# Optimization experiments

Measured on AMD Instinct MI355X. Metric: run time of the kernel, lower is better.

Reference implementation:

```python
import jax, jax.numpy as jnp
import numpy as np

B, C, HEADS, DH = 2, 1280, 20, 64
INNER = HEADS * DH
HW = 64
S = HW * HW
L = 77
ENC = 4096
GROUPS = 32
EPS = 1e-5
CREG = 1.0     # creg_ in __init__
NOATTN = 1.0   # global noattn
NORES = 1.0    # global noresidual


def setup_inputs() -> dict:
    key = jax.random.key(0)
    ks = jax.random.split(key, 10)
    std = 0.02
    return {
        "x": jax.random.normal(ks[0], (B, C, HW, HW), jnp.float32),
        "text": jax.random.normal(ks[1], (B, L, ENC), jnp.float32),
        "gn_gamma": jnp.ones((C,), jnp.float32),
        "gn_beta": jnp.zeros((C,), jnp.float32),
        "ln_gamma": jnp.ones((ENC,), jnp.float32),
        "ln_beta": jnp.zeros((ENC,), jnp.float32),
        "Wq": jax.random.normal(ks[2], (C, INNER), jnp.float32) * std,
        "bq": jnp.zeros((INNER,), jnp.float32),
        "Wk": jax.random.normal(ks[3], (ENC, INNER), jnp.float32) * std,
        "bk": jnp.zeros((INNER,), jnp.float32),
        "Wv": jax.random.normal(ks[4], (ENC, INNER), jnp.float32) * std,
        "bv": jnp.zeros((INNER,), jnp.float32),
        "Wo": jax.random.normal(ks[5], (INNER, C), jnp.float32) * std,
        "bo": jnp.zeros((C,), jnp.float32),
        "size_reg": jax.random.uniform(ks[6], (1, S, L), jnp.float32),
        "treg": jax.random.uniform(ks[7], (1,), jnp.float32),
        "mask": jax.random.randint(ks[8], (1, S, L), 0, 2, jnp.int32),
    }


def _group_norm(h, gamma, beta):
    # h: [B, C, S]; GroupNorm over (C//GROUPS, S) per group
    hg = h.reshape(B, GROUPS, -1)
    mu = hg.mean(-1, keepdims=True)
    var = hg.var(-1, keepdims=True)
    hn = ((hg - mu) * jax.lax.rsqrt(var + EPS)).reshape(B, C, S)
    return hn * gamma[None, :, None] + beta[None, :, None]


def _layer_norm(t, gamma, beta):
    mu = t.mean(-1, keepdims=True)
    var = t.var(-1, keepdims=True)
    return (t - mu) * jax.lax.rsqrt(var + EPS) * gamma + beta


def reference(x, text, gn_gamma, gn_beta, ln_gamma, ln_beta, Wq, bq, Wk, bk,
              Wv, bv, Wo, bo, size_reg, treg, mask):
    residual = x                              # [B, C, HW, HW]
    h = x.reshape(B, C, S)                    # spatial tokens
    h = _group_norm(h, gn_gamma, gn_beta).transpose(0, 2, 1)   # [B, S, C]
    enc = _layer_norm(text, ln_gamma, ln_beta)                  # [B, L, ENC]

    # head_to_batch_dim (out_dim=3): [B, T, inner] -> [B*heads, T, dh]
    q = (h @ Wq + bq).reshape(B, S, HEADS, DH).transpose(0, 2, 1, 3).reshape(B * HEADS, S, DH)
    k = (enc @ Wk + bk).reshape(B, L, HEADS, DH).transpose(0, 2, 1, 3).reshape(B * HEADS, L, DH)
    v = (enc @ Wv + bv).reshape(B, L, HEADS, DH).transpose(0, 2, 1, 3).reshape(B * HEADS, L, DH)

    scale = DH ** -0.5
    sim = jnp.einsum('bsd,bld->bsl', q, k) * scale            # [B*H, S, L]

    # region regularization applied only to the conditional (second) half
    half = (B * HEADS) // 2
    sim_u, sim_c = sim[:half], sim[half:]
    mn = sim_c.min(-1, keepdims=True)
    mx = sim_c.max(-1, keepdims=True)
    m = mask > 0                                               # [1, S, L] broadcasts over heads
    w = size_reg * CREG * treg[0]
    sim_c = sim_c + jnp.where(m, w, 0.0) * (mx - sim_c) - jnp.where(m, 0.0, w) * (sim_c - mn)
    sim = jnp.concatenate([sim_u, sim_c], axis=0)

    probs = jax.nn.softmax(sim, axis=-1)
    out = jnp.einsum('bsl,bld->bsd', probs, v)                 # [B*H, S, DH]
    # batch_to_head_dim: [B*H, S, DH] -> [B, S, inner]
    out = out.reshape(B, HEADS, S, DH).transpose(0, 2, 1, 3).reshape(B, S, INNER)
    out = out @ Wo + bo                                        # to_out[0]; dropout p=0
    out = out.transpose(0, 2, 1).reshape(residual.shape)       # [B, C, HW, HW]
    return out * NOATTN + residual * NORES
```

## Files before the change

### kernel.cpp

```cpp
#include <hip/hip_runtime.h>

typedef __bf16 bf16_t;
typedef __bf16 bf16x8 __attribute__((ext_vector_type(8)));
typedef float  f32x4  __attribute__((ext_vector_type(4)));
typedef unsigned int u32x4 __attribute__((ext_vector_type(4)));


__global__ __launch_bounds__(256) void k_transpose_cvt2(
    const float* __restrict__ in0, const float* __restrict__ in1,
    bf16_t* __restrict__ out0, bf16_t* __restrict__ out1, int R, int C)
{
  const float* in  = blockIdx.z ? in1 : in0;
  bf16_t*      out = blockIdx.z ? out1 : out0;
  __shared__ float tile[64][33];
  const int c0 = blockIdx.x * 32, r0 = blockIdx.y * 64;
  const int t = threadIdx.x;
#pragma unroll
  for (int it = 0; it < 8; ++it) {
    int r = it * 8 + (t >> 5), c = t & 31;
    tile[r][c] = in[(size_t)(r0 + r) * C + c0 + c];
  }
  __syncthreads();
  {
    const int oc  = t >> 3;
    const int seg = t & 7;
    bf16x8 o;
#pragma unroll
    for (int e = 0; e < 8; ++e) o[e] = (bf16_t)tile[seg * 8 + e][oc];
    *(bf16x8*)(out + (size_t)(c0 + oc) * R + r0 + seg * 8) = o;
  }
}

__global__ __launch_bounds__(256) void k_gn_partial(
    const float* __restrict__ x, float* __restrict__ partial)
{
  const int bg    = blockIdx.x >> 5;
  const int chunk = blockIdx.x & 31;
  const float* p  = x + (size_t)bg * 163840 + (size_t)chunk * 5120;
  float s1 = 0.f, s2 = 0.f;
#pragma unroll
  for (int it = 0; it < 5; ++it) {
    float4 v = *(const float4*)(p + (size_t)(it * 256 + threadIdx.x) * 4);
    s1 += v.x + v.y + v.z + v.w;
    s2 += v.x * v.x + v.y * v.y + v.z * v.z + v.w * v.w;
  }
#pragma unroll
  for (int off = 32; off > 0; off >>= 1) {
    s1 += __shfl_down(s1, off);
    s2 += __shfl_down(s2, off);
  }
  __shared__ float r1[4], r2[4];
  if ((threadIdx.x & 63) == 0) { r1[threadIdx.x >> 6] = s1; r2[threadIdx.x >> 6] = s2; }
  __syncthreads();
  if (threadIdx.x == 0) {
    partial[blockIdx.x * 2]     = r1[0] + r1[1] + r1[2] + r1[3];
    partial[blockIdx.x * 2 + 1] = r2[0] + r2[1] + r2[2] + r2[3];
  }
}

__global__ __launch_bounds__(64) void k_gn_finalize(
    const float* __restrict__ partial, float* __restrict__ stats)
{
  const int bg = threadIdx.x;
  float t1 = 0.f, t2 = 0.f;
#pragma unroll
  for (int c = 0; c < 32; ++c) {
    t1 += partial[(bg * 32 + c) * 2];
    t2 += partial[(bg * 32 + c) * 2 + 1];
  }
  const float invN = 1.0f / 163840.0f;
  float mu  = t1 * invN;
  float var = t2 * invN - mu * mu;
  stats[bg * 2]     = mu;
  stats[bg * 2 + 1] = rsqrtf(var + 1e-5f);
}

__global__ __launch_bounds__(256) void k_gn_apply(
    const float* __restrict__ x, const float* __restrict__ stats,
    const float* __restrict__ gamma, const float* __restrict__ beta,
    bf16_t* __restrict__ h)
{
  __shared__ float tile[64][65];
  const int s0 = blockIdx.x * 64;
  const int c0 = blockIdx.y * 64;
  const int b  = blockIdx.z;
  const int t  = threadIdx.x;
#pragma unroll
  for (int it = 0; it < 16; ++it) {
    int cl = it * 4 + (t >> 6);
    int sl = t & 63;
    tile[cl][sl] = x[((size_t)(b * 1280 + c0 + cl) << 12) + s0 + sl];
  }
  __syncthreads();
#pragma unroll
  for (int it = 0; it < 2; ++it) {
    int i  = it * 256 + t;
    int sl = i >> 3;
    int cg = i & 7;
    bf16x8 o;
#pragma unroll
    for (int e = 0; e < 8; ++e) {
      int c  = c0 + cg * 8 + e;
      int g  = c / 40;
      float mu = stats[(b * 32 + g) * 2];
      float rs = stats[(b * 32 + g) * 2 + 1];
      o[e] = (bf16_t)((tile[cg * 8 + e][sl] - mu) * rs * gamma[c] + beta[c]);
    }
    *(bf16x8*)(h + (size_t)(b * 4096 + s0 + sl) * 1280 + c0 + cg * 8) = o;
  }
}

__global__ __launch_bounds__(256) void k_ln(
    const float* __restrict__ text, const float* __restrict__ g,
    const float* __restrict__ bta, bf16_t* __restrict__ enc)
{
  const int row = blockIdx.x;
  const float* p = text + (size_t)row * 4096;
  float s1 = 0.f, s2 = 0.f;
  for (int i = threadIdx.x; i < 1024; i += 256) {
    float4 v = *(const float4*)(p + (size_t)i * 4);
    s1 += v.x + v.y + v.z + v.w;
    s2 += v.x * v.x + v.y * v.y + v.z * v.z + v.w * v.w;
  }
#pragma unroll
  for (int off = 32; off > 0; off >>= 1) {
    s1 += __shfl_down(s1, off);
    s2 += __shfl_down(s2, off);
  }
  __shared__ float r1[4], r2[4], sh[2];
  if ((threadIdx.x & 63) == 0) { r1[threadIdx.x >> 6] = s1; r2[threadIdx.x >> 6] = s2; }
  __syncthreads();
  if (threadIdx.x == 0) {
    float t1 = r1[0] + r1[1] + r1[2] + r1[3];
    float t2 = r2[0] + r2[1] + r2[2] + r2[3];
    const float invN = 1.0f / 4096.0f;
    float mu  = t1 * invN;
    float var = t2 * invN - mu * mu;
    sh[0] = mu;
    sh[1] = rsqrtf(var + 1e-5f);
  }
  __syncthreads();
  const float mu = sh[0], rs = sh[1];
  for (int i = threadIdx.x; i < 1024; i += 256) {
    float4 v  = *(const float4*)(p + (size_t)i * 4);
    float4 gg = *(const float4*)(g + (size_t)i * 4);
    float4 bb = *(const float4*)(bta + (size_t)i * 4);
    bf16_t* o = enc + (size_t)row * 4096 + (size_t)i * 4;
    o[0] = (bf16_t)((v.x - mu) * rs * gg.x + bb.x);
    o[1] = (bf16_t)((v.y - mu) * rs * gg.y + bb.y);
    o[2] = (bf16_t)((v.z - mu) * rs * gg.z + bb.z);
    o[3] = (bf16_t)((v.w - mu) * rs * gg.w + bb.w);
  }
}

template <int EPI>
__global__ __launch_bounds__(256, 3) void k_gemm(
    const bf16_t* __restrict__ A, const bf16_t* __restrict__ BT,
    const float* __restrict__ bias, bf16_t* __restrict__ outb,
    float* __restrict__ outf, const float* __restrict__ xres,
    float* __restrict__ dout, int M, int lda, int klen, int nnt, int nst)
{
  __shared__ alignas(16) bf16_t smem[24576];
  const int tid  = threadIdx.x;
  const int lane = tid & 63;
  const int wv   = tid >> 6;
  const int wm   = wv >> 1, wn = wv & 1;

  const int cpx  = gridDim.x >> 3;
  const int nbid = (blockIdx.x & 7) * cpx + (blockIdx.x >> 3);
  const int mt   = nbid / nnt, ntile = nbid % nnt;
  const int m0   = mt * 128;
  const int n0   = ntile * 64;
  const int kbeg = blockIdx.z * klen;

  f32x4 acc[4][2];
  const f32x4 fz = {0.f, 0.f, 0.f, 0.f};
#pragma unroll
  for (int i = 0; i < 4; ++i)
#pragma unroll
    for (int j = 0; j < 2; ++j) acc[i][j] = fz;

  auto stage = [&](int buf, int kt) {
    bf16_t* sA = smem + buf * 8192;
    bf16_t* sB = smem + 16384 + buf * 4096;
#pragma unroll
    for (int it = 0; it < 4; ++it) {
      int slot = it * 256 + tid;
      int row  = slot >> 3, ch = slot & 7;
      int grow = m0 + row; if (grow > M - 1) grow = M - 1;
      const bf16_t* ga = A + (size_t)grow * lda + kt + ((ch ^ (row & 7)) << 3);
      __builtin_amdgcn_global_load_lds(
          (const __attribute__((address_space(1))) void*)ga,
          (__attribute__((address_space(3))) void*)((char*)sA + slot * 16),
          16, 0, 0);
    }
#pragma unroll
    for (int it = 0; it < 2; ++it) {
      int slot = it * 256 + tid;
      int row  = slot >> 3, ch = slot & 7;
      const bf16_t* gb = BT + (size_t)(n0 + row) * lda + kt + ((ch ^ (row & 7)) << 3);
      __builtin_amdgcn_global_load_lds(
          (const __attribute__((address_space(1))) void*)gb,
          (__attribute__((address_space(3))) void*)((char*)sB + slot * 16),
          16, 0, 0);
    }
  };

  const int nt_k = klen >> 6;
  stage(0, kbeg);
  if (nt_k > 1) stage(1, kbeg + 64);

  for (int t = 0; t < nt_k; ++t) {
    if (t + 1 < nt_k) { asm volatile("s_waitcnt vmcnt(6)" ::: "memory"); }
    else              { asm volatile("s_waitcnt vmcnt(0)" ::: "memory"); }
    __builtin_amdgcn_s_barrier();
    const char* pA = (const char*)(smem + (t & 1) * 8192);
    const char* pB = (const char*)(smem + 16384 + (t & 1) * 4096);
#pragma unroll
    for (int ks = 0; ks < 2; ++ks) {
      const int kb = ks * 64 + ((lane >> 4) << 4);
      bf16x8 af[4], bfg[2];
#pragma unroll
      for (int i = 0; i < 4; ++i) {
        int r = wm * 64 + i * 16 + (lane & 15);
        af[i] = *(const bf16x8*)(pA + r * 128 + (kb ^ ((r & 7) << 4)));
      }
#pragma unroll
      for (int j = 0; j < 2; ++j) {
        int c = wn * 32 + j * 16 + (lane & 15);
        bfg[j] = *(const bf16x8*)(pB + c * 128 + (kb ^ ((c & 7) << 4)));
      }
#pragma unroll
      for (int i = 0; i < 4; ++i)
#pragma unroll
        for (int j = 0; j < 2; ++j)
          acc[i][j] = __builtin_amdgcn_mfma_f32_16x16x32_bf16(af[i], bfg[j], acc[i][j], 0, 0, 0);
    }
    asm volatile("s_waitcnt lgkmcnt(0)" ::: "memory");
    __builtin_amdgcn_s_barrier();
    if (t + 2 < nt_k) stage(t & 1, kbeg + (t + 2) * 64);
  }

  if (EPI == 0) {
    bf16_t* cst = smem;
#pragma unroll
    for (int j = 0; j < 2; ++j) {
      const int n  = n0 + wn * 32 + j * 16 + (lane & 15);
      const float bs = bias[n];
      const int cl = wn * 32 + j * 16 + (lane & 15);
#pragma unroll
      for (int i = 0; i < 4; ++i) {
        const int rl = wm * 64 + i * 16 + ((lane >> 4) << 2);
#pragma unroll
        for (int r = 0; r < 4; ++r)
          cst[(rl + r) * 76 + cl] = (bf16_t)(acc[i][j][r] + bs);
      }
    }
    __syncthreads();
#pragma unroll
    for (int it = 0; it < 4; ++it) {
      int slot = it * 256 + tid;
      int row = slot >> 3, ch = slot & 7;
      u32x4 d = *(const u32x4*)(cst + row * 76 + ch * 8);
      *(u32x4*)(outb + (size_t)(m0 + row) * 1280 + n0 + ch * 8) = d;
    }
  } else {
#pragma unroll
    for (int i = 0; i < 4; ++i) {
      const int mrow = m0 + wm * 64 + i * 16 + ((lane >> 4) << 2);
#pragma unroll
      for (int j = 0; j < 2; ++j) {
        const int n = n0 + wn * 32 + j * 16 + (lane & 15);
        if (EPI == 2) {
          const int b = mrow >> 12, s = mrow & 4095;
          const size_t off = ((size_t)(b * 1280 + n) << 12) + s;
          const float bs = bias[n];
          const float4 xr = *(const float4*)(xres + off);
          float4 o;
          o.x = acc[i][j][0] + bs + xr.x;
          o.y = acc[i][j][1] + bs + xr.y;
          o.z = acc[i][j][2] + bs + xr.z;
          o.w = acc[i][j][3] + bs + xr.w;
          *(float4*)(dout + off) = o;
        } else {
#pragma unroll
          for (int r = 0; r < 4; ++r)
            if (mrow + r < M)
              outf[(size_t)blockIdx.z * 154 * nst + (size_t)(mrow + r) * nst + n] = acc[i][j][r];
        }
      }
    }
  }
}

__global__ __launch_bounds__(256) void k_kv_reduce(
    const float* __restrict__ part, const float* __restrict__ bk,
    const float* __restrict__ bv, bf16_t* __restrict__ kb, bf16_t* __restrict__ vb)
{
  const int idx = blockIdx.x * 256 + threadIdx.x;
  if (idx >= 154 * 2560) return;
  const int r = idx / 2560, n = idx % 2560;
  float s = (n < 1280) ? bk[n] : bv[n - 1280];
#pragma unroll
  for (int sp = 0; sp < 8; ++sp) s += part[(size_t)sp * (154 * 2560) + idx];
  if (n < 1280) kb[(size_t)r * 1280 + n] = (bf16_t)s;
  else          vb[(size_t)r * 1280 + n - 1280] = (bf16_t)s;
}

__global__ __launch_bounds__(256) void k_attn(
    const bf16_t* __restrict__ q, const bf16_t* __restrict__ kbuf,
    const bf16_t* __restrict__ vbuf, bf16_t* __restrict__ ao,
    const float* __restrict__ size_reg, const int* __restrict__ mask,
    const float* __restrict__ treg)
{
  __shared__ alignas(16) bf16_t sQ[64 * 64];
  __shared__ alignas(16) bf16_t sK[80 * 64];
  __shared__ alignas(16) bf16_t sVT[64 * 104];
  __shared__ alignas(16) bf16_t sP[4 * 16 * 104];
  const int s0   = blockIdx.x * 64;
  const int bh   = blockIdx.y;
  const int b    = bh / 20, head = bh % 20;
  const int tid  = threadIdx.x, lane = tid & 63, wv = tid >> 6;
  const int ntok = lane & 15;

  const u32x4 uz = {0u, 0u, 0u, 0u};
  for (int i = tid; i < 832; i += 256) ((u32x4*)sVT)[i] = uz;
  for (int i = tid; i < 832; i += 256) ((u32x4*)sP)[i]  = uz;

  const size_t qbase = ((size_t)(b * 4096 + s0)) * 1280 + head * 64;
  for (int slot = tid; slot < 512; slot += 256) {
    int row = slot >> 3, ch = slot & 7;
    u32x4 d = *(const u32x4*)(q + qbase + (size_t)row * 1280 + ((ch ^ (row & 7)) << 3));
    *(u32x4*)((char*)sQ + slot * 16) = d;
  }
  const size_t kvbase = ((size_t)(b * 77)) * 1280 + head * 64;
  for (int slot = tid; slot < 640; slot += 256) {
    int tok = slot >> 3, ch = slot & 7;
    u32x4 d = uz;
    if (tok < 77)
      d = *(const u32x4*)(kbuf + kvbase + (size_t)tok * 1280 + ((ch ^ (tok & 7)) << 3));
    *(u32x4*)((char*)sK + slot * 16) = d;
  }
  __syncthreads();
  for (int e = tid; e < 77 * 64; e += 256) {
    int tok = e >> 6, dh = e & 63;
    sVT[dh * 104 + tok] = vbuf[kvbase + (size_t)tok * 1280 + dh];
  }
  __syncthreads();

  f32x4 sim[5];
  const f32x4 fz = {0.f, 0.f, 0.f, 0.f};
#pragma unroll
  for (int nf = 0; nf < 5; ++nf) sim[nf] = fz;
  const int qrow = wv * 16 + (lane & 15);
#pragma unroll
  for (int ks = 0; ks < 2; ++ks) {
    const int kb = ks * 64 + ((lane >> 4) << 4);
    bf16x8 aq = *(const bf16x8*)((const char*)sQ + qrow * 128 + (kb ^ ((qrow & 7) << 4)));
#pragma unroll
    for (int nf = 0; nf < 5; ++nf) {
      int tok = nf * 16 + ntok;
      bf16x8 bk = *(const bf16x8*)((const char*)sK + tok * 128 + (kb ^ ((tok & 7) << 4)));
      sim[nf] = __builtin_amdgcn_mfma_f32_16x16x32_bf16(aq, bk, sim[nf], 0, 0, 0);
    }
  }

  float vv[5][4];
#pragma unroll
  for (int nf = 0; nf < 5; ++nf)
#pragma unroll
    for (int r = 0; r < 4; ++r) vv[nf][r] = sim[nf][r] * 0.125f;

  const int rbase = s0 + wv * 16 + ((lane >> 4) << 2);

  if (b == 1) {
    const float tr = treg[0];
#pragma unroll
    for (int r = 0; r < 4; ++r) {
      float mx = -1e30f, mn = 1e30f;
#pragma unroll
      for (int nf = 0; nf < 5; ++nf)
        if (nf * 16 + ntok < 77) { mx = fmaxf(mx, vv[nf][r]); mn = fminf(mn, vv[nf][r]); }
#pragma unroll
      for (int m = 1; m < 16; m <<= 1) {
        mx = fmaxf(mx, __shfl_xor(mx, m));
        mn = fminf(mn, __shfl_xor(mn, m));
      }
      const int srow = rbase + r;
#pragma unroll
      for (int nf = 0; nf < 5; ++nf) {
        int l = nf * 16 + ntok;
        if (l < 77) {
          float w  = size_reg[srow * 77 + l] * tr;
          int   mk = mask[srow * 77 + l];
          float v  = vv[nf][r];
          vv[nf][r] = (mk > 0) ? v + w * (mx - v) : v - w * (v - mn);
        }
      }
    }
  }

#pragma unroll
  for (int r = 0; r < 4; ++r) {
    float mx = -1e30f;
#pragma unroll
    for (int nf = 0; nf < 5; ++nf)
      if (nf * 16 + ntok < 77) mx = fmaxf(mx, vv[nf][r]);
#pragma unroll
    for (int m = 1; m < 16; m <<= 1) mx = fmaxf(mx, __shfl_xor(mx, m));
    float p[5]; float sm = 0.f;
#pragma unroll
    for (int nf = 0; nf < 5; ++nf) {
      bool val = (nf * 16 + ntok) < 77;
      p[nf] = val ? __expf(vv[nf][r] - mx) : 0.f;
      sm += p[nf];
    }
#pragma unroll
    for (int m = 1; m < 16; m <<= 1) sm += __shfl_xor(sm, m);
    const float inv = 1.0f / sm;
    const int prow = ((lane >> 4) << 2) + r;
#pragma unroll
    for (int nf = 0; nf < 5; ++nf)
      sP[wv * 1664 + prow * 104 + nf * 16 + ntok] = (bf16_t)(p[nf] * inv);
  }
  __syncthreads();

  f32x4 o[4];
#pragma unroll
  for (int fd = 0; fd < 4; ++fd) o[fd] = fz;
#pragma unroll
  for (int ks = 0; ks < 3; ++ks) {
    const int kb = ks * 64 + ((lane >> 4) << 4);
    bf16x8 ap = *(const bf16x8*)((const char*)sP + wv * 3328 + (lane & 15) * 208 + kb);
#pragma unroll
    for (int fd = 0; fd < 4; ++fd) {
      bf16x8 bv = *(const bf16x8*)((const char*)sVT + (fd * 16 + (lane & 15)) * 208 + kb);
      o[fd] = __builtin_amdgcn_mfma_f32_16x16x32_bf16(ap, bv, o[fd], 0, 0, 0);
    }
  }
  const size_t obase =
      ((size_t)(b * 4096 + s0 + wv * 16 + ((lane >> 4) << 2))) * 1280 + head * 64;
#pragma unroll
  for (int fd = 0; fd < 4; ++fd)
#pragma unroll
    for (int r = 0; r < 4; ++r)
      ao[obase + (size_t)r * 1280 + fd * 16 + (lane & 15)] = (bf16_t)o[fd][r];
}

extern "C" void kernel_launch(void* const* d_in, const int* in_sizes, int n_in,
                              void* d_out, int out_size, void* d_ws, size_t ws_size,
                              hipStream_t stream)
{
  const float* x    = (const float*)d_in[0];
  const float* text = (const float*)d_in[1];
  const float* gng  = (const float*)d_in[2];
  const float* gnb  = (const float*)d_in[3];
  const float* lng  = (const float*)d_in[4];
  const float* lnb  = (const float*)d_in[5];
  const float* Wq   = (const float*)d_in[6];
  const float* bq   = (const float*)d_in[7];
  const float* Wk   = (const float*)d_in[8];
  const float* bk   = (const float*)d_in[9];
  const float* Wv   = (const float*)d_in[10];
  const float* bv   = (const float*)d_in[11];
  const float* Wo   = (const float*)d_in[12];
  const float* bo   = (const float*)d_in[13];
  const float* sreg = (const float*)d_in[14];
  const float* treg = (const float*)d_in[15];
  const int*   msk  = (const int*)d_in[16];
  float* out = (float*)d_out;

  char* ws = (char*)d_ws;
  size_t off = 0;
  auto alloc = [&](size_t bytes) {
    char* p = ws + off;
    off += (bytes + 255) & ~(size_t)255;
    return p;
  };
  float*  partial = (float*)alloc(2048 * 2 * sizeof(float));
  float*  stats   = (float*)alloc(64 * 2 * sizeof(float));
  bf16_t* WqT = (bf16_t*)alloc((size_t)1280 * 1280 * 2);
  bf16_t* WkT = (bf16_t*)alloc((size_t)1280 * 4096 * 2);
  bf16_t* WvT = (bf16_t*)alloc((size_t)1280 * 4096 * 2);
  bf16_t* WoT = (bf16_t*)alloc((size_t)1280 * 1280 * 2);
  bf16_t* h   = (bf16_t*)alloc((size_t)8192 * 1280 * 2);
  bf16_t* enc = (bf16_t*)alloc((size_t)154 * 4096 * 2);
  bf16_t* qb  = (bf16_t*)alloc((size_t)8192 * 1280 * 2);
  bf16_t* kb  = (bf16_t*)alloc((size_t)154 * 1280 * 2);
  bf16_t* vb  = (bf16_t*)alloc((size_t)154 * 1280 * 2);
  float*  part = (float*)alloc((size_t)8 * 154 * 2560 * sizeof(float));

  k_transpose_cvt2<<<dim3(40, 20, 2), 256, 0, stream>>>(Wq, Wo, WqT, WoT, 1280, 1280);
  k_transpose_cvt2<<<dim3(40, 64, 2), 256, 0, stream>>>(Wk, Wv, WkT, WvT, 4096, 1280);

  k_gn_partial<<<2048, 256, 0, stream>>>(x, partial);
  k_gn_finalize<<<1, 64, 0, stream>>>(partial, stats);
  k_gn_apply<<<dim3(64, 20, 2), 256, 0, stream>>>(x, stats, gng, gnb, h);
  k_ln<<<154, 256, 0, stream>>>(text, lng, lnb, enc);

  k_gemm<0><<<dim3(1280), 256, 0, stream>>>(h, WqT, bq, qb, nullptr, nullptr, nullptr,
                                            8192, 1280, 1280, 20, 1280);
  k_gemm<1><<<dim3(80, 1, 8), 256, 0, stream>>>(enc, WkT, nullptr, nullptr, part, nullptr, nullptr,
                                                154, 4096, 512, 40, 2560);
  k_kv_reduce<<<1540, 256, 0, stream>>>(part, bk, bv, kb, vb);

  k_attn<<<dim3(64, 40), 256, 0, stream>>>(qb, kb, vb, h, sreg, msk, treg);

  k_gemm<2><<<dim3(1280), 256, 0, stream>>>(h, WoT, bo, nullptr, nullptr, x, out,
                                            8192, 1280, 1280, 20, 1280);
}
```

Baseline: 175.1 us.

## Load GEMM B-operand straight into registers and shrink LDS for higher occupancy

The Q-projection and output-projection GEMMs get a new kernel that stages only the A tile in LDS through global_load_lds. Each wave loads its B (weight) fragments directly from global memory into double-buffered registers, one k-step ahead. This cuts LDS use from 48KB to 32KB and raises the launch-bounds occupancy hint from 3 to 4 blocks per CU. The cost is uncoalesced per-lane B loads and more register pressure; the K/V GEMM keeps the old split-K kernel.

```diff
diff --git a/kernel.cpp b/kernel.cpp
--- a/kernel.cpp
+++ b/kernel.cpp
@@ -154,11 +154,144 @@
 }
 
 template <int EPI>
-__global__ __launch_bounds__(256, 3) void k_gemm(
+__global__ __launch_bounds__(256, 4) void k_gemm_breg(
     const bf16_t* __restrict__ A, const bf16_t* __restrict__ BT,
     const float* __restrict__ bias, bf16_t* __restrict__ outb,
-    float* __restrict__ outf, const float* __restrict__ xres,
-    float* __restrict__ dout, int M, int lda, int klen, int nnt, int nst)
+    const float* __restrict__ xres, float* __restrict__ dout,
+    int M, int lda, int klen, int nnt)
+{
+  __shared__ alignas(16) bf16_t smem[16384];
+  const int tid  = threadIdx.x;
+  const int lane = tid & 63;
+  const int wv   = tid >> 6;
+  const int wm   = wv >> 1, wn = wv & 1;
+
+  const int cpx  = gridDim.x >> 3;
+  const int nbid = (blockIdx.x & 7) * cpx + (blockIdx.x >> 3);
+  const int mt   = nbid / nnt, ntile = nbid % nnt;
+  const int m0   = mt * 128;
+  const int n0   = ntile * 64;
+
+  f32x4 acc[4][2];
+  const f32x4 fz = {0.f, 0.f, 0.f, 0.f};
+#pragma unroll
+  for (int i = 0; i < 4; ++i)
+#pragma unroll
+    for (int j = 0; j < 2; ++j) acc[i][j] = fz;
+
+  const bf16_t* bbase =
+      BT + (size_t)(n0 + wn * 32 + (lane & 15)) * lda + ((lane >> 4) << 3);
+
+  auto stageA = [&](int buf, int kt) {
+    bf16_t* sA = smem + buf * 8192;
+#pragma unroll
+    for (int it = 0; it < 4; ++it) {
+      int slot = it * 256 + tid;
+      int row  = slot >> 3, ch = slot & 7;
+      const bf16_t* ga = A + (size_t)(m0 + row) * lda + kt + ((ch ^ (row & 7)) << 3);
+      __builtin_amdgcn_global_load_lds(
+          (const __attribute__((address_space(1))) void*)ga,
+          (__attribute__((address_space(3))) void*)((char*)sA + slot * 16),
+          16, 0, 0);
+    }
+  };
+
+#define LOADB(DST, KT)                                                         \
+  {                                                                            \
+    _Pragma("unroll") for (int j = 0; j < 2; ++j)                              \
+        _Pragma("unroll") for (int ks = 0; ks < 2; ++ks)                       \
+            DST[j * 2 + ks] =                                                  \
+        *(const bf16x8*)(bbase + (size_t)j * 16 * lda + (KT) + ks * 32);       \
+  }
+
+  const int nt_k = klen >> 6;
+  bf16x8 b0[4], b1[4];
+  stageA(0, 0);
+  LOADB(b0, 0);
+  if (nt_k > 1) stageA(1, 64);
+
+#define GEMM_STEP(T, BCUR, BNXT)                                               \
+  {                                                                            \
+    if ((T) + 1 < nt_k) { asm volatile("s_waitcnt vmcnt(8)" ::: "memory"); }   \
+    else                { asm volatile("s_waitcnt vmcnt(0)" ::: "memory"); }   \
+    __builtin_amdgcn_s_barrier();                                              \
+    if ((T) + 1 < nt_k) LOADB(BNXT, ((T) + 1) * 64);                           \
+    const char* pA = (const char*)(smem + ((T) & 1) * 8192);                   \
+    _Pragma("unroll") for (int ks = 0; ks < 2; ++ks) {                         \
+      const int kb = ks * 64 + ((lane >> 4) << 4);                             \
+      bf16x8 af[4];                                                            \
+      _Pragma("unroll") for (int i = 0; i < 4; ++i) {                          \
+        int r = wm * 64 + i * 16 + (lane & 15);                                \
+        af[i] = *(const bf16x8*)(pA + r * 128 + (kb ^ ((r & 7) << 4)));        \
+      }                                                                        \
+      _Pragma("unroll") for (int i = 0; i < 4; ++i)                            \
+        _Pragma("unroll") for (int j = 0; j < 2; ++j)                          \
+          acc[i][j] = __builtin_amdgcn_mfma_f32_16x16x32_bf16(                 \
+              af[i], BCUR[j * 2 + ks], acc[i][j], 0, 0, 0);                    \
+    }                                                                          \
+    asm volatile("s_waitcnt lgkmcnt(0)" ::: "memory");                         \
+    __builtin_amdgcn_s_barrier();                                              \
+    if ((T) + 2 < nt_k) stageA((T) & 1, ((T) + 2) * 64);                       \
+  }
+
+  int t = 0;
+  for (; t + 1 < nt_k; t += 2) {
+    GEMM_STEP(t, b0, b1);
+    GEMM_STEP(t + 1, b1, b0);
+  }
+  if (t < nt_k) GEMM_STEP(t, b0, b1);
+
+#undef GEMM_STEP
+#undef LOADB
+
+  if (EPI == 0) {
+    bf16_t* cst = smem;
+#pragma unroll
+    for (int j = 0; j < 2; ++j) {
+      const int n  = n0 + wn * 32 + j * 16 + (lane & 15);
+      const float bs = bias[n];
+      const int cl = wn * 32 + j * 16 + (lane & 15);
+#pragma unroll
+      for (int i = 0; i < 4; ++i) {
+        const int rl = wm * 64 + i * 16 + ((lane >> 4) << 2);
+#pragma unroll
+        for (int r = 0; r < 4; ++r)
+          cst[(rl + r) * 76 + cl] = (bf16_t)(acc[i][j][r] + bs);
+      }
+    }
+    __syncthreads();
+#pragma unroll
+    for (int it = 0; it < 4; ++it) {
+      int slot = it * 256 + tid;
+      int row = slot >> 3, ch = slot & 7;
+      u32x4 d = *(const u32x4*)(cst + row * 76 + ch * 8);
+      *(u32x4*)(outb + (size_t)(m0 + row) * 1280 + n0 + ch * 8) = d;
+    }
+  } else {
+#pragma unroll
+    for (int i = 0; i < 4; ++i) {
+      const int mrow = m0 + wm * 64 + i * 16 + ((lane >> 4) << 2);
+#pragma unroll
+      for (int j = 0; j < 2; ++j) {
+        const int n = n0 + wn * 32 + j * 16 + (lane & 15);
+        const int b = mrow >> 12, s = mrow & 4095;
+        const size_t off = ((size_t)(b * 1280 + n) << 12) + s;
+        const float bs = bias[n];
+        const float4 xr = *(const float4*)(xres + off);
+        float4 o;
+        o.x = acc[i][j][0] + bs + xr.x;
+        o.y = acc[i][j][1] + bs + xr.y;
+        o.z = acc[i][j][2] + bs + xr.z;
+        o.w = acc[i][j][3] + bs + xr.w;
+        *(float4*)(dout + off) = o;
+      }
+    }
+  }
+}
+
+__global__ __launch_bounds__(256, 3) void k_gemm_kv(
+    const bf16_t* __restrict__ A, const bf16_t* __restrict__ BT,
+    float* __restrict__ outf, int M, int lda, int klen, int nnt, int nst)
 {
   __shared__ alignas(16) bf16_t smem[24576];
   const int tid  = threadIdx.x;
@@ -241,54 +374,16 @@
     if (t + 2 < nt_k) stage(t & 1, kbeg + (t + 2) * 64);
   }
 
-  if (EPI == 0) {
-    bf16_t* cst = smem;
+#pragma unroll
+  for (int i = 0; i < 4; ++i) {
+    const int mrow = m0 + wm * 64 + i * 16 + ((lane >> 4) << 2);
 #pragma unroll
     for (int j = 0; j < 2; ++j) {
-      const int n  = n0 + wn * 32 + j * 16 + (lane & 15);
-      const float bs = bias[n];
-      const int cl = wn * 32 + j * 16 + (lane & 15);
-#pragma unroll
-      for (int i = 0; i < 4; ++i) {
-        const int rl = wm * 64 + i * 16 + ((lane >> 4) << 2);
-#pragma unroll
-        for (int r = 0; r < 4; ++r)
-          cst[(rl + r) * 76 + cl] = (bf16_t)(acc[i][j][r] + bs);
-      }
-    }
-    __syncthreads();
-#pragma unroll
-    for (int it = 0; it < 4; ++it) {
-      int slot = it * 256 + tid;
-      int row = slot >> 3, ch = slot & 7;
-      u32x4 d = *(const u32x4*)(cst + row * 76 + ch * 8);
-      *(u32x4*)(outb + (size_t)(m0 + row) * 1280 + n0 + ch * 8) = d;
-    }
-  } else {
-#pragma unroll
-    for (int i = 0; i < 4; ++i) {
-      const int mrow = m0 + wm * 64 + i * 16 + ((lane >> 4) << 2);
-#pragma unroll
-      for (int j = 0; j < 2; ++j) {
-        const int n = n0 + wn * 32 + j * 16 + (lane & 15);
-        if (EPI == 2) {
-          const int b = mrow >> 12, s = mrow & 4095;
-          const size_t off = ((size_t)(b * 1280 + n) << 12) + s;
-          const float bs = bias[n];
-          const float4 xr = *(const float4*)(xres + off);
-          float4 o;
-          o.x = acc[i][j][0] + bs + xr.x;
-          o.y = acc[i][j][1] + bs + xr.y;
-          o.z = acc[i][j][2] + bs + xr.z;
-          o.w = acc[i][j][3] + bs + xr.w;
-          *(float4*)(dout + off) = o;
-        } else {
-#pragma unroll
-          for (int r = 0; r < 4; ++r)
-            if (mrow + r < M)
-              outf[(size_t)blockIdx.z * 154 * nst + (size_t)(mrow + r) * nst + n] = acc[i][j][r];
-        }
-      }
+      const int n = n0 + wn * 32 + j * 16 + (lane & 15);
+#pragma unroll
+      for (int r = 0; r < 4; ++r)
+        if (mrow + r < M)
+          outf[(size_t)blockIdx.z * 154 * nst + (size_t)(mrow + r) * nst + n] = acc[i][j][r];
     }
   }
 }
@@ -498,14 +593,13 @@
   k_gn_apply<<<dim3(64, 20, 2), 256, 0, stream>>>(x, stats, gng, gnb, h);
   k_ln<<<154, 256, 0, stream>>>(text, lng, lnb, enc);
 
-  k_gemm<0><<<dim3(1280), 256, 0, stream>>>(h, WqT, bq, qb, nullptr, nullptr, nullptr,
-                                            8192, 1280, 1280, 20, 1280);
-  k_gemm<1><<<dim3(80, 1, 8), 256, 0, stream>>>(enc, WkT, nullptr, nullptr, part, nullptr, nullptr,
-                                                154, 4096, 512, 40, 2560);
+  k_gemm_breg<0><<<dim3(1280), 256, 0, stream>>>(h, WqT, bq, qb, nullptr, nullptr,
+                                                 8192, 1280, 1280, 20);
+  k_gemm_kv<<<dim3(80, 1, 8), 256, 0, stream>>>(enc, WkT, part, 154, 4096, 512, 40, 2560);
   k_kv_reduce<<<1540, 256, 0, stream>>>(part, bk, bv, kb, vb);
 
   k_attn<<<dim3(64, 40), 256, 0, stream>>>(qb, kb, vb, h, sreg, msk, treg);
 
-  k_gemm<2><<<dim3(1280), 256, 0, stream>>>(h, WoT, bo, nullptr, nullptr, x, out,
-                                            8192, 1280, 1280, 20, 1280);
-}
+  k_gemm_breg<2><<<dim3(1280), 256, 0, stream>>>(h, WoT, bo, nullptr, x, out,
+                                                 8192, 1280, 1280, 20);
+}
```

Measured after the change: 241.9 us. 1.38x slower.

## Use 256x64 GEMM tiles for Q and output projections; merge weight transposes

Applied to the files above, without the earlier changes.

Adds a dedicated big-tile GEMM kernel (256 rows by 64 columns per block, each wave owning 64 rows by 64 columns, 4x4 MFMA accumulators) for the Q projection and the output projection with residual. It keeps the old 128x64 kernel only for the split-K KV GEMM. The larger tiles double A/B reuse per LDS load and halve the block count, at the cost of more LDS and registers (occupancy bound drops to 2). The two weight transpose launches are also merged into one four-way launch, which trims launch overhead but adds idle early-exit blocks.

```diff
diff --git a/kernel.cpp b/kernel.cpp
--- a/kernel.cpp
+++ b/kernel.cpp
@@ -6,19 +6,25 @@
 typedef unsigned int u32x4 __attribute__((ext_vector_type(4)));
 
 
-__global__ __launch_bounds__(256) void k_transpose_cvt2(
-    const float* __restrict__ in0, const float* __restrict__ in1,
-    bf16_t* __restrict__ out0, bf16_t* __restrict__ out1, int R, int C)
-{
-  const float* in  = blockIdx.z ? in1 : in0;
-  bf16_t*      out = blockIdx.z ? out1 : out0;
+__global__ __launch_bounds__(256) void k_transpose_cvt4(
+    const float* __restrict__ w0, const float* __restrict__ w1,
+    const float* __restrict__ w2, const float* __restrict__ w3,
+    bf16_t* __restrict__ o0, bf16_t* __restrict__ o1,
+    bf16_t* __restrict__ o2, bf16_t* __restrict__ o3)
+{
+  const int z = blockIdx.z;
+  const float* in  = (z == 0) ? w0 : (z == 1) ? w1 : (z == 2) ? w2 : w3;
+  bf16_t*      out = (z == 0) ? o0 : (z == 1) ? o1 : (z == 2) ? o2 : o3;
+  const int R = (z < 2) ? 1280 : 4096;
+  const int r0 = blockIdx.y * 64;
+  if (r0 >= R) return;
   __shared__ float tile[64][33];
-  const int c0 = blockIdx.x * 32, r0 = blockIdx.y * 64;
+  const int c0 = blockIdx.x * 32;
   const int t = threadIdx.x;
 #pragma unroll
   for (int it = 0; it < 8; ++it) {
     int r = it * 8 + (t >> 5), c = t & 31;
-    tile[r][c] = in[(size_t)(r0 + r) * C + c0 + c];
+    tile[r][c] = in[(size_t)(r0 + r) * 1280 + c0 + c];
   }
   __syncthreads();
   {
@@ -154,11 +160,138 @@
 }
 
 template <int EPI>
-__global__ __launch_bounds__(256, 3) void k_gemm(
+__global__ __launch_bounds__(256, 2) void k_gemm_big(
     const bf16_t* __restrict__ A, const bf16_t* __restrict__ BT,
     const float* __restrict__ bias, bf16_t* __restrict__ outb,
-    float* __restrict__ outf, const float* __restrict__ xres,
-    float* __restrict__ dout, int M, int lda, int klen, int nnt, int nst)
+    const float* __restrict__ xres, float* __restrict__ dout,
+    int lda, int klen, int nnt)
+{
+  __shared__ alignas(16) bf16_t smem[40960];
+  const int tid  = threadIdx.x;
+  const int lane = tid & 63;
+  const int wv   = tid >> 6;
+
+  const int cpx  = gridDim.x >> 3;
+  const int nbid = (blockIdx.x & 7) * cpx + (blockIdx.x >> 3);
+  const int mt   = nbid / nnt, ntile = nbid % nnt;
+  const int m0   = mt * 256;
+  const int n0   = ntile * 64;
+
+  f32x4 acc[4][4];
+  const f32x4 fz = {0.f, 0.f, 0.f, 0.f};
+#pragma unroll
+  for (int i = 0; i < 4; ++i)
+#pragma unroll
+    for (int j = 0; j < 4; ++j) acc[i][j] = fz;
+
+  auto stage = [&](int buf, int kt) {
+    bf16_t* sA = smem + buf * 16384;
+    bf16_t* sB = smem + 32768 + buf * 4096;
+#pragma unroll
+    for (int it = 0; it < 8; ++it) {
+      int slot = it * 256 + tid;
+      int row  = slot >> 3, ch = slot & 7;
+      const bf16_t* ga = A + (size_t)(m0 + row) * lda + kt + ((ch ^ (row & 7)) << 3);
+      __builtin_amdgcn_global_load_lds(
+          (const __attribute__((address_space(1))) void*)ga,
+          (__attribute__((address_space(3))) void*)((char*)sA + slot * 16),
+          16, 0, 0);
+    }
+#pragma unroll
+    for (int it = 0; it < 2; ++it) {
+      int slot = it * 256 + tid;
+      int row  = slot >> 3, ch = slot & 7;
+      const bf16_t* gb = BT + (size_t)(n0 + row) * lda + kt + ((ch ^ (row & 7)) << 3);
+      __builtin_amdgcn_global_load_lds(
+          (const __attribute__((address_space(1))) void*)gb,
+          (__attribute__((address_space(3))) void*)((char*)sB + slot * 16),
+          16, 0, 0);
+    }
+  };
+
+  const int nt_k = klen >> 6;
+  stage(0, 0);
+  if (nt_k > 1) stage(1, 64);
+
+  for (int t = 0; t < nt_k; ++t) {
+    if (t + 1 < nt_k) { asm volatile("s_waitcnt vmcnt(10)" ::: "memory"); }
+    else              { asm volatile("s_waitcnt vmcnt(0)" ::: "memory"); }
+    __builtin_amdgcn_s_barrier();
+    const char* pA = (const char*)(smem + (t & 1) * 16384);
+    const char* pB = (const char*)(smem + 32768 + (t & 1) * 4096);
+#pragma unroll
+    for (int ks = 0; ks < 2; ++ks) {
+      const int kb = ks * 64 + ((lane >> 4) << 4);
+      bf16x8 af[4], bfg[4];
+#pragma unroll
+      for (int i = 0; i < 4; ++i) {
+        int r = wv * 64 + i * 16 + (lane & 15);
+        af[i] = *(const bf16x8*)(pA + r * 128 + (kb ^ ((r & 7) << 4)));
+      }
+#pragma unroll
+      for (int j = 0; j < 4; ++j) {
+        int c = j * 16 + (lane & 15);
+        bfg[j] = *(const bf16x8*)(pB + c * 128 + (kb ^ ((c & 7) << 4)));
+      }
+#pragma unroll
+      for (int i = 0; i < 4; ++i)
+#pragma unroll
+        for (int j = 0; j < 4; ++j)
+          acc[i][j] = __builtin_amdgcn_mfma_f32_16x16x32_bf16(af[i], bfg[j], acc[i][j], 0, 0, 0);
+    }
+    asm volatile("s_waitcnt lgkmcnt(0)" ::: "memory");
+    __builtin_amdgcn_s_barrier();
+    if (t + 2 < nt_k) stage(t & 1, (t + 2) * 64);
+  }
+
+  if (EPI == 0) {
+    bf16_t* cst = smem;
+#pragma unroll
+    for (int j = 0; j < 4; ++j) {
+      const int n  = n0 + j * 16 + (lane & 15);
+      const float bs = bias[n];
+      const int cl = j * 16 + (lane & 15);
+#pragma unroll
+      for (int i = 0; i < 4; ++i) {
+        const int rl = wv * 64 + i * 16 + ((lane >> 4) << 2);
+#pragma unroll
+        for (int r = 0; r < 4; ++r)
+          cst[(rl + r) * 76 + cl] = (bf16_t)(acc[i][j][r] + bs);
+      }
+    }
+    __syncthreads();
+#pragma unroll
+    for (int it = 0; it < 8; ++it) {
+      int slot = it * 256 + tid;
+      int row = slot >> 3, ch = slot & 7;
+      u32x4 d = *(const u32x4*)(cst + row * 76 + ch * 8);
+      *(u32x4*)(outb + (size_t)(m0 + row) * 1280 + n0 + ch * 8) = d;
+    }
+  } else {
+#pragma unroll
+    for (int i = 0; i < 4; ++i) {
+      const int mrow = m0 + wv * 64 + i * 16 + ((lane >> 4) << 2);
+#pragma unroll
+      for (int j = 0; j < 4; ++j) {
+        const int n = n0 + j * 16 + (lane & 15);
+        const int b = mrow >> 12, s = mrow & 4095;
+        const size_t off = ((size_t)(b * 1280 + n) << 12) + s;
+        const float bs = bias[n];
+        const float4 xr = *(const float4*)(xres + off);
+        float4 o;
+        o.x = acc[i][j][0] + bs + xr.x;
+        o.y = acc[i][j][1] + bs + xr.y;
+        o.z = acc[i][j][2] + bs + xr.z;
+        o.w = acc[i][j][3] + bs + xr.w;
+        *(float4*)(dout + off) = o;
+      }
+    }
+  }
+}
+
+__global__ __launch_bounds__(256, 3) void k_gemm_kv(
+    const bf16_t* __restrict__ A, const bf16_t* __restrict__ BT,
+    float* __restrict__ outf, int M, int lda, int klen, int nnt, int nst)
 {
   __shared__ alignas(16) bf16_t smem[24576];
   const int tid  = threadIdx.x;
@@ -241,54 +374,16 @@
     if (t + 2 < nt_k) stage(t & 1, kbeg + (t + 2) * 64);
   }
 
-  if (EPI == 0) {
-    bf16_t* cst = smem;
+#pragma unroll
+  for (int i = 0; i < 4; ++i) {
+    const int mrow = m0 + wm * 64 + i * 16 + ((lane >> 4) << 2);
 #pragma unroll
     for (int j = 0; j < 2; ++j) {
-      const int n  = n0 + wn * 32 + j * 16 + (lane & 15);
-      const float bs = bias[n];
-      const int cl = wn * 32 + j * 16 + (lane & 15);
-#pragma unroll
-      for (int i = 0; i < 4; ++i) {
-        const int rl = wm * 64 + i * 16 + ((lane >> 4) << 2);
-#pragma unroll
-        for (int r = 0; r < 4; ++r)
-          cst[(rl + r) * 76 + cl] = (bf16_t)(acc[i][j][r] + bs);
-      }
-    }
-    __syncthreads();
-#pragma unroll
-    for (int it = 0; it < 4; ++it) {
-      int slot = it * 256 + tid;
-      int row = slot >> 3, ch = slot & 7;
-      u32x4 d = *(const u32x4*)(cst + row * 76 + ch * 8);
-      *(u32x4*)(outb + (size_t)(m0 + row) * 1280 + n0 + ch * 8) = d;
-    }
-  } else {
-#pragma unroll
-    for (int i = 0; i < 4; ++i) {
-      const int mrow = m0 + wm * 64 + i * 16 + ((lane >> 4) << 2);
-#pragma unroll
-      for (int j = 0; j < 2; ++j) {
-        const int n = n0 + wn * 32 + j * 16 + (lane & 15);
-        if (EPI == 2) {
-          const int b = mrow >> 12, s = mrow & 4095;
-          const size_t off = ((size_t)(b * 1280 + n) << 12) + s;
-          const float bs = bias[n];
-          const float4 xr = *(const float4*)(xres + off);
-          float4 o;
-          o.x = acc[i][j][0] + bs + xr.x;
-          o.y = acc[i][j][1] + bs + xr.y;
-          o.z = acc[i][j][2] + bs + xr.z;
-          o.w = acc[i][j][3] + bs + xr.w;
-          *(float4*)(dout + off) = o;
-        } else {
-#pragma unroll
-          for (int r = 0; r < 4; ++r)
-            if (mrow + r < M)
-              outf[(size_t)blockIdx.z * 154 * nst + (size_t)(mrow + r) * nst + n] = acc[i][j][r];
-        }
-      }
+      const int n = n0 + wn * 32 + j * 16 + (lane & 15);
+#pragma unroll
+      for (int r = 0; r < 4; ++r)
+        if (mrow + r < M)
+          outf[(size_t)blockIdx.z * 154 * nst + (size_t)(mrow + r) * nst + n] = acc[i][j][r];
     }
   }
 }
@@ -490,22 +585,21 @@
   bf16_t* vb  = (bf16_t*)alloc((size_t)154 * 1280 * 2);
   float*  part = (float*)alloc((size_t)8 * 154 * 2560 * sizeof(float));
 
-  k_transpose_cvt2<<<dim3(40, 20, 2), 256, 0, stream>>>(Wq, Wo, WqT, WoT, 1280, 1280);
-  k_transpose_cvt2<<<dim3(40, 64, 2), 256, 0, stream>>>(Wk, Wv, WkT, WvT, 4096, 1280);
+  k_transpose_cvt4<<<dim3(40, 64, 4), 256, 0, stream>>>(Wq, Wo, Wk, Wv,
+                                                        WqT, WoT, WkT, WvT);
 
   k_gn_partial<<<2048, 256, 0, stream>>>(x, partial);
   k_gn_finalize<<<1, 64, 0, stream>>>(partial, stats);
   k_gn_apply<<<dim3(64, 20, 2), 256, 0, stream>>>(x, stats, gng, gnb, h);
   k_ln<<<154, 256, 0, stream>>>(text, lng, lnb, enc);
 
-  k_gemm<0><<<dim3(1280), 256, 0, stream>>>(h, WqT, bq, qb, nullptr, nullptr, nullptr,
-                                            8192, 1280, 1280, 20, 1280);
-  k_gemm<1><<<dim3(80, 1, 8), 256, 0, stream>>>(enc, WkT, nullptr, nullptr, part, nullptr, nullptr,
-                                                154, 4096, 512, 40, 2560);
+  k_gemm_big<0><<<dim3(640), 256, 0, stream>>>(h, WqT, bq, qb, nullptr, nullptr,
+                                               1280, 1280, 20);
+  k_gemm_kv<<<dim3(80, 1, 8), 256, 0, stream>>>(enc, WkT, part, 154, 4096, 512, 40, 2560);
   k_kv_reduce<<<1540, 256, 0, stream>>>(part, bk, bv, kb, vb);
 
   k_attn<<<dim3(64, 40), 256, 0, stream>>>(qb, kb, vb, h, sreg, msk, treg);
 
-  k_gemm<2><<<dim3(1280), 256, 0, stream>>>(h, WoT, bo, nullptr, nullptr, x, out,
-                                            8192, 1280, 1280, 20, 1280);
-}
+  k_gemm_big<2><<<dim3(640), 256, 0, stream>>>(h, WoT, bo, nullptr, x, out,
+                                               1280, 1280, 20);
+}
```

Result: slower. 183.0 us (+4.5%).
